# Kernel tuning notes

Hardware: AMD Instinct MI355X
Metric: run time of the kernel (lower is better)

The kernel has to match this reference:

```python
import jax, jax.numpy as jnp
import numpy as np

BSZ, SEQ, T, ENC, HID = 32, 2048, 32, 512, 512


def setup_inputs() -> dict:
    key = jax.random.key(0)
    ks = jax.random.split(key, 8)
    L = SEQ // T  # uniform turn length -> end ids cover every token
    end_ids = jnp.broadcast_to((jnp.arange(T, dtype=jnp.int32) + 1) * L - 1, (BSZ, T))
    s = 1.0 / np.sqrt(HID)
    return {
        "encoder_output": jax.random.normal(ks[0], (BSZ, SEQ, ENC), jnp.float32),
        "end_ids": end_ids,
        "W_ih": jax.random.uniform(ks[1], (4 * HID, ENC), jnp.float32, -s, s),
        "W_hh": jax.random.uniform(ks[2], (4 * HID, HID), jnp.float32, -s, s),
        "b_ih": jax.random.uniform(ks[3], (4 * HID,), jnp.float32, -s, s),
        "b_hh": jax.random.uniform(ks[4], (4 * HID,), jnp.float32, -s, s),
        "fc_w": jax.random.uniform(ks[5], (1, HID + ENC), jnp.float32, -s, s),
        "fc_b": jnp.zeros((1,), jnp.float32),
    }


def reference(encoder_output, end_ids, W_ih, W_hh, b_ih, b_hh, fc_w, fc_b):
    bsz, S, E = encoder_output.shape
    Tn = end_ids.shape[1]
    H = W_hh.shape[1]

    # ---- ragged segment-mean pooling: token t in turn j iff prev_end < t <= end[j]
    tok = jnp.arange(S)
    seg = jax.vmap(lambda e: jnp.searchsorted(e, tok))(end_ids)  # [bsz,S]
    gid = (seg + jnp.arange(bsz)[:, None] * Tn).reshape(-1)
    sums = jax.ops.segment_sum(encoder_output.reshape(-1, E), gid, num_segments=bsz * Tn)
    starts = jnp.concatenate([jnp.zeros((bsz, 1), end_ids.dtype), end_ids[:, :-1] + 1], axis=1)
    counts = (end_ids - starts + 1).astype(encoder_output.dtype)  # [bsz,Tn]
    turn_states = sums.reshape(bsz, Tn, E) / counts[..., None]

    # ---- all sliding windows of 3 consecutive turns
    J = Tn - 3
    widx = jnp.arange(J)[:, None] + jnp.arange(3)[None, :]  # [J,3]
    src = turn_states[:, widx].reshape(bsz * J, 3, E)  # [N,3,E]

    # ---- single-layer LSTM (pytorch gate order i,f,g,o), take last hidden state
    bias = b_ih + b_hh

    def step(carry, x_t):
        h, c = carry
        g = x_t @ W_ih.T + h @ W_hh.T + bias
        i_, f_, g_, o_ = jnp.split(g, 4, axis=-1)
        c = jax.nn.sigmoid(f_) * c + jax.nn.sigmoid(i_) * jnp.tanh(g_)
        h = jax.nn.sigmoid(o_) * jnp.tanh(c)
        return (h, c), None

    h0 = jnp.zeros((bsz * J, H), src.dtype)
    (hT, _), _ = jax.lax.scan(step, (h0, h0), jnp.swapaxes(src, 0, 1))

    # ---- con_fc([src_last, tgt]) decomposes into src-part + tgt-part of the weight
    sscore = (hT @ fc_w[0, :H]).reshape(bsz, J)  # [bsz,J]
    tscore = turn_states @ fc_w[0, H:]  # [bsz,Tn]
    kidx = jnp.arange(J)[:, None] + 3 + jnp.arange(J)[None, :]  # [J,J] candidate turn ids
    valid = kidx < Tn
    kc = jnp.clip(kidx, 0, Tn - 1)
    logits = sscore[:, :, None] + tscore[:, kc] + fc_b[0]  # [bsz,J,J]
    logits = jnp.where(valid[None], logits, jnp.float32(-1e9))
    # cross entropy with target index 0 (the j+3 turn is the positive)
    loss = jax.nn.logsumexp(logits, axis=-1) - logits[..., 0]  # [bsz,J]
    return jnp.mean(loss)
```

## Files before the change

kernel.cpp:

```cpp
#include <hip/hip_runtime.h>
#include <math.h>

#define BSZ   32
#define SEQL  2048
#define TN    32
#define ENCD  512
#define HIDD  512
#define JW    29
#define NW    (BSZ * JW)

typedef short bf16x8 __attribute__((ext_vector_type(8)));
typedef float f32x4  __attribute__((ext_vector_type(4)));

__device__ __forceinline__ float sigm(float x) { return 1.f / (1.f + expf(-x)); }

__device__ __forceinline__ unsigned short f2bf(float x) {
    union { float f; unsigned u; } v; v.f = x;
    unsigned u = v.u;
    u += 0x7FFF + ((u >> 16) & 1);
    return (unsigned short)(u >> 16);
}
__device__ __forceinline__ float bf2f(short s) {
    union { unsigned u; float f; } v; v.u = ((unsigned)(unsigned short)s) << 16;
    return v.f;
}

#define GLOAD_LDS16(gp, lp)                                                    \
    __builtin_amdgcn_global_load_lds(                                          \
        (const __attribute__((address_space(1))) void*)(gp),                   \
        (__attribute__((address_space(3))) void*)(lp), 16, 0, 0)

__global__ __launch_bounds__(512) void prep_k(const float* __restrict__ enc,
                                              const int* __restrict__ end_ids,
                                              short* __restrict__ tsbf,
                                              const float* __restrict__ w1,
                                              const float* __restrict__ w2,
                                              short* __restrict__ o1,
                                              short* __restrict__ o2,
                                              const float* __restrict__ fcw,
                                              float* __restrict__ tsc) {
    int tid = threadIdx.x;
    int bid = blockIdx.x;
    if (bid >= 1024) {
        int idx = (bid - 1024) * 512 + tid;
        int t = idx >> 17;
        int i = idx & 131071;
        const float* s = (t ? w2 : w1) + (size_t)i * 8;
        short* o = (t ? o2 : o1) + (size_t)i * 8;
        float4 a = ((const float4*)s)[0];
        float4 b = ((const float4*)s)[1];
        union { short v[8]; bf16x8 p; } r;
        r.v[0] = (short)f2bf(a.x); r.v[1] = (short)f2bf(a.y);
        r.v[2] = (short)f2bf(a.z); r.v[3] = (short)f2bf(a.w);
        r.v[4] = (short)f2bf(b.x); r.v[5] = (short)f2bf(b.y);
        r.v[6] = (short)f2bf(b.z); r.v[7] = (short)f2bf(b.w);
        *(bf16x8*)o = r.p;
        return;
    }
    int j = bid & 31;
    int b = bid >> 5;
    int e_end   = end_ids[bid];
    int e_start = j ? (end_ids[bid - 1] + 1) : 0;
    int col = (tid & 127) << 2;
    int tr  = tid >> 7;
    const float* base = enc + (size_t)b * SEQL * ENCD + col;
    float ax = 0.f, ay = 0.f, az = 0.f, aw = 0.f;
    float bx = 0.f, by = 0.f, bz = 0.f, bw = 0.f;
    for (int t = e_start + tr; t <= e_end; t += 8) {
        float4 v = *(const float4*)(base + (size_t)t * ENCD);
        ax += v.x; ay += v.y; az += v.z; aw += v.w;
        int t2 = t + 4;
        if (t2 <= e_end) {
            float4 u = *(const float4*)(base + (size_t)t2 * ENCD);
            bx += u.x; by += u.y; bz += u.z; bw += u.w;
        }
    }
    ax += bx; ay += by; az += bz; aw += bw;
    __shared__ float4 part[3][128];
    __shared__ float red[128];
    if (tr) part[tr - 1][tid & 127] = make_float4(ax, ay, az, aw);
    __syncthreads();
    if (!tr) {
        float4 p0 = part[0][tid], p1 = part[1][tid], p2 = part[2][tid];
        float inv = 1.f / (float)(e_end - e_start + 1);
        float mx = (ax + p0.x + p1.x + p2.x) * inv;
        float my = (ay + p0.y + p1.y + p2.y) * inv;
        float mz = (az + p0.z + p1.z + p2.z) * inv;
        float mw = (aw + p0.w + p1.w + p2.w) * inv;
        union { unsigned short v[4]; uint2 p; } q;
        q.v[0] = f2bf(mx); q.v[1] = f2bf(my); q.v[2] = f2bf(mz); q.v[3] = f2bf(mw);
        *(uint2*)(tsbf + (size_t)bid * ENCD + col) = q.p;
        float4 wv = *(const float4*)(fcw + HIDD + col);
        red[tid] = mx * wv.x + my * wv.y + mz * wv.z + mw * wv.w;
    }
    __syncthreads();
    if (tid < 64) {
        float s = red[tid] + red[tid + 64];
#pragma unroll
        for (int sh = 32; sh; sh >>= 1) s += __shfl_down(s, sh, 64);
        if (tid == 0) tsc[bid] = s;
    }
}

template <int STEP>
__global__ __launch_bounds__(256, 2) void gemm_lstm(const short* __restrict__ A,
                                                 const short* __restrict__ B,
                                                 ushort4* __restrict__ XWq,
                                                 float* __restrict__ Cb,
                                                 short* __restrict__ Hout,
                                                 float* __restrict__ ss_part,
                                                 const float* __restrict__ b_ih,
                                                 const float* __restrict__ b_hh,
                                                 const float* __restrict__ fcw) {
    __shared__ short Bpanel[64 * 512];
    __shared__ short Als[2][64 * 64];
    int tid = threadIdx.x, w = tid >> 6, lane = tid & 63;
    int l15 = lane & 15, l4 = lane >> 4;
    int m0 = blockIdx.y * 64, hcol0 = blockIdx.x * 16;
    int hcol = hcol0 + l15;
    const short* Aptr = A + (size_t)m0 * 512;

#pragma unroll
    for (int i = 0; i < 16; ++i) {
        int r = w * 16 + i;
        int grow = (r >> 4) * 512 + hcol0 + (r & 15);
        int scol = lane ^ (r & 7);
        GLOAD_LDS16(B + (size_t)grow * 512 + scol * 8, &Bpanel[r * 512]);
    }
    auto stageA = [&](int sel, int k0) {
#pragma unroll
        for (int i = 0; i < 2; ++i) {
            int c = w * 2 + i;
            int unit = c * 64 + lane;
            int row = unit >> 3, slot = unit & 7;
            int scol = slot ^ (row & 7);
            GLOAD_LDS16(Aptr + (size_t)row * 512 + k0 + scol * 8,
                        &Als[sel][c * 512]);
        }
    };
    stageA(0, 0);
    __syncthreads();

    f32x4 acc[4] = {};
    int sel = 0;
    for (int t = 0; t < 8; ++t) {
        if (t < 7) stageA(sel ^ 1, (t + 1) * 64);
        bf16x8 af[2], bfr[4][2];
#pragma unroll
        for (int kk = 0; kk < 2; ++kk) {
            int row = w * 16 + l15;
            int s = (kk * 4 + l4) ^ (row & 7);
            af[kk] = *(const bf16x8*)&Als[sel][row * 64 + s * 8];
#pragma unroll
            for (int g = 0; g < 4; ++g) {
                int rr = g * 16 + l15;
                int s2 = t * 8 + ((kk * 4 + l4) ^ (rr & 7));
                bfr[g][kk] = *(const bf16x8*)&Bpanel[rr * 512 + s2 * 8];
            }
        }
#pragma unroll
        for (int kk = 0; kk < 2; ++kk)
#pragma unroll
            for (int g = 0; g < 4; ++g)
                acc[g] = __builtin_amdgcn_mfma_f32_16x16x32_bf16(
                    af[kk], bfr[g][kk], acc[g], 0, 0, 0);
        __syncthreads();
        sel ^= 1;
    }

    float bb0, bb1, bb2, bb3;
    if (STEP == 1) {
        bb0 = b_ih[hcol]        + b_hh[hcol];
        bb1 = b_ih[512 + hcol]  + b_hh[512 + hcol];
        bb2 = b_ih[1024 + hcol] + b_hh[1024 + hcol];
        bb3 = b_ih[1536 + hcol] + b_hh[1536 + hcol];
    }
    float hreg[4];
#pragma unroll
    for (int r = 0; r < 4; ++r) {
        int row = m0 + w * 16 + l4 * 4 + r;
        float gi = acc[0][r], gf = acc[1][r];
        float gg = acc[2][r], go = acc[3][r];
        float cn;
        if (STEP == 1) {
            gi += bb0; gf += bb1; gg += bb2; go += bb3;
            ushort4 q;
            q.x = f2bf(gi); q.y = f2bf(gf); q.z = f2bf(gg); q.w = f2bf(go);
            XWq[(size_t)row * 512 + hcol] = q;
            cn = sigm(gi) * tanhf(gg);
        } else {
            int xr = row + (STEP - 1); if (xr > 1023) xr = 1023;
            ushort4 q = XWq[(size_t)xr * 512 + hcol];
            gi += bf2f((short)q.x); gf += bf2f((short)q.y);
            gg += bf2f((short)q.z); go += bf2f((short)q.w);
            cn = sigm(gf) * Cb[(size_t)row * 512 + hcol] + sigm(gi) * tanhf(gg);
        }
        float h = sigm(go) * tanhf(cn);
        if (STEP < 3) {
            Cb[(size_t)row * 512 + hcol] = cn;
            Hout[(size_t)row * 512 + hcol] = (short)f2bf(h);
        } else {
            hreg[r] = h;
        }
    }
    if (STEP == 3) {
        float fcv = fcw[hcol];
#pragma unroll
        for (int r = 0; r < 4; ++r) {
            float v = hreg[r] * fcv;
#pragma unroll
            for (int m = 1; m < 16; m <<= 1) v += __shfl_xor(v, m, 64);
            if (l15 == 0) {
                int row = m0 + w * 16 + l4 * 4 + r;
                ss_part[(size_t)row * 32 + blockIdx.x] = v;
            }
        }
    }
}

__global__ __launch_bounds__(1024) void loss_k(const float* __restrict__ ss_part,
                                               const float* __restrict__ tsc,
                                               const float* __restrict__ fcb,
                                               float* __restrict__ out) {
    int tid = threadIdx.x;
    float l = 0.f;
    if (tid < NW) {
        int b = tid / JW, j = tid - (tid / JW) * JW;
        int turn = b * TN + j;
        const float* sp = ss_part + (size_t)turn * 32;
        float s = 0.f;
#pragma unroll
        for (int k = 0; k < 32; ++k) s += sp[k];
        float base = s + fcb[0];
        int nv = JW - j;
        const float* tp = tsc + b * TN + j + 3;
        float m = -1e30f, l0 = 0.f;
        for (int k = 0; k < nv; ++k) {
            float lg = base + tp[k];
            if (k == 0) l0 = lg;
            m = fmaxf(m, lg);
        }
        float sum = 0.f;
        for (int k = 0; k < nv; ++k) sum += expf(base + tp[k] - m);
        l = (m + logf(sum)) - l0;
    }
    __shared__ float red[16];
#pragma unroll
    for (int s = 32; s; s >>= 1) l += __shfl_down(l, s, 64);
    int wid = tid >> 6, lane = tid & 63;
    if (lane == 0) red[wid] = l;
    __syncthreads();
    if (tid == 0) {
        float tot = 0.f;
        for (int i = 0; i < 16; ++i) tot += red[i];
        out[0] = tot / (float)NW;
    }
}

extern "C" void kernel_launch(void* const* d_in, const int* in_sizes, int n_in,
                              void* d_out, int out_size, void* d_ws, size_t ws_size,
                              hipStream_t stream) {
    const float* enc     = (const float*)d_in[0];
    const int*   end_ids = (const int*)d_in[1];
    const float* W_ih    = (const float*)d_in[2];
    const float* W_hh    = (const float*)d_in[3];
    const float* b_ih    = (const float*)d_in[4];
    const float* b_hh    = (const float*)d_in[5];
    const float* fc_w    = (const float*)d_in[6];
    const float* fc_b    = (const float*)d_in[7];
    float* out = (float*)d_out;

    short* tsbf   = (short*)d_ws;
    short* Wih_bf = tsbf + 1024 * 512;
    short* Whh_bf = Wih_bf + 2048 * 512;
    short* HA     = Whh_bf + 2048 * 512;
    short* HB     = HA + 1024 * 512;
    ushort4* XWq  = (ushort4*)(HB + 1024 * 512);
    float* Cb     = (float*)(XWq + 1024 * 512);
    float* ss_part = Cb + 1024 * 512;
    float* tsc    = ss_part + 1024 * 32;

    prep_k<<<1536, 512, 0, stream>>>(enc, end_ids, tsbf, W_ih, W_hh,
                                     Wih_bf, Whh_bf, fc_w, tsc);
    gemm_lstm<1><<<dim3(32, 16), 256, 0, stream>>>(tsbf, Wih_bf, XWq, Cb, HA,
                                                   nullptr, b_ih, b_hh, fc_w);
    gemm_lstm<2><<<dim3(32, 16), 256, 0, stream>>>(HA, Whh_bf, XWq, Cb, HB,
                                                   nullptr, b_ih, b_hh, fc_w);
    gemm_lstm<3><<<dim3(32, 16), 256, 0, stream>>>(HB, Whh_bf, XWq, Cb, nullptr,
                                                   ss_part, b_ih, b_hh, fc_w);
    loss_k<<<1, 1024, 0, stream>>>(ss_part, tsc, fc_b, out);
}
```

Before: 67.51 us.

## Load LSTM GEMM A operand directly into registers, drop LDS double-buffer

The A-operand tile is no longer staged through a double-buffered LDS array. Each lane now loads its full 512-wide row slice into registers up front, so the main loop has no per-iteration __syncthreads. The launch-bounds occupancy hint of 2 blocks per CU is removed, which allows higher register use (64 extra VGPRs for areg) at the possible cost of occupancy. Global loads are now 16-byte per lane with row strides, instead of async LDS copies, and they all issue before the loop.

```diff
diff --git a/kernel.cpp b/kernel.cpp
--- a/kernel.cpp
+++ b/kernel.cpp
@@ -103,7 +103,7 @@
 }
 
 template <int STEP>
-__global__ __launch_bounds__(256, 2) void gemm_lstm(const short* __restrict__ A,
+__global__ __launch_bounds__(256) void gemm_lstm(const short* __restrict__ A,
                                                  const short* __restrict__ B,
                                                  ushort4* __restrict__ XWq,
                                                  float* __restrict__ Cb,
@@ -113,12 +113,19 @@
                                                  const float* __restrict__ b_hh,
                                                  const float* __restrict__ fcw) {
     __shared__ short Bpanel[64 * 512];
-    __shared__ short Als[2][64 * 64];
     int tid = threadIdx.x, w = tid >> 6, lane = tid & 63;
     int l15 = lane & 15, l4 = lane >> 4;
     int m0 = blockIdx.y * 64, hcol0 = blockIdx.x * 16;
     int hcol = hcol0 + l15;
-    const short* Aptr = A + (size_t)m0 * 512;
+
+    int arow = m0 + w * 16 + l15;
+    const short* Arow = A + (size_t)arow * 512;
+    bf16x8 areg[8][2];
+#pragma unroll
+    for (int t = 0; t < 8; ++t)
+#pragma unroll
+        for (int kk = 0; kk < 2; ++kk)
+            areg[t][kk] = *(const bf16x8*)(Arow + t * 64 + (kk * 4 + l4) * 8);
 
 #pragma unroll
     for (int i = 0; i < 16; ++i) {
@@ -127,45 +134,26 @@
         int scol = lane ^ (r & 7);
         GLOAD_LDS16(B + (size_t)grow * 512 + scol * 8, &Bpanel[r * 512]);
     }
-    auto stageA = [&](int sel, int k0) {
-#pragma unroll
-        for (int i = 0; i < 2; ++i) {
-            int c = w * 2 + i;
-            int unit = c * 64 + lane;
-            int row = unit >> 3, slot = unit & 7;
-            int scol = slot ^ (row & 7);
-            GLOAD_LDS16(Aptr + (size_t)row * 512 + k0 + scol * 8,
-                        &Als[sel][c * 512]);
-        }
-    };
-    stageA(0, 0);
     __syncthreads();
 
     f32x4 acc[4] = {};
-    int sel = 0;
+#pragma unroll
     for (int t = 0; t < 8; ++t) {
-        if (t < 7) stageA(sel ^ 1, (t + 1) * 64);
-        bf16x8 af[2], bfr[4][2];
-#pragma unroll
-        for (int kk = 0; kk < 2; ++kk) {
-            int row = w * 16 + l15;
-            int s = (kk * 4 + l4) ^ (row & 7);
-            af[kk] = *(const bf16x8*)&Als[sel][row * 64 + s * 8];
+        bf16x8 bfr[4][2];
+#pragma unroll
+        for (int kk = 0; kk < 2; ++kk)
 #pragma unroll
             for (int g = 0; g < 4; ++g) {
                 int rr = g * 16 + l15;
                 int s2 = t * 8 + ((kk * 4 + l4) ^ (rr & 7));
                 bfr[g][kk] = *(const bf16x8*)&Bpanel[rr * 512 + s2 * 8];
             }
-        }
 #pragma unroll
         for (int kk = 0; kk < 2; ++kk)
 #pragma unroll
             for (int g = 0; g < 4; ++g)
                 acc[g] = __builtin_amdgcn_mfma_f32_16x16x32_bf16(
-                    af[kk], bfr[g][kk], acc[g], 0, 0, 0);
-        __syncthreads();
-        sel ^= 1;
+                    areg[t][kk], bfr[g][kk], acc[g], 0, 0, 0);
     }
 
     float bb0, bb1, bb2, bb3;
```

New measurement: 69.95 us. 3.6% more time.
